# Performance work log

Hardware: AMD Instinct MI355X
Metric: run time of the kernel (lower is better)

Reference implementation:

```python
import jax, jax.numpy as jnp
import numpy as np

EMBED = 512
HEADS = 8
HEAD_DIM = EMBED // HEADS
MLP_HIDDEN = EMBED * 4
EPS = 1e-5


def _layernorm(x, g, b):
    mu = jnp.mean(x, axis=-1, keepdims=True)
    var = jnp.var(x, axis=-1, keepdims=True)
    return (x - mu) * jax.lax.rsqrt(var + EPS) * g + b


def setup_inputs() -> dict:
    key = jax.random.key(0)
    ks = jax.random.split(key, 12)
    s = 0.02
    return {
        "x": jax.random.normal(ks[0], (4, 2048, EMBED), dtype=jnp.float32),
        "ln1_g": jnp.ones((EMBED,), jnp.float32),
        "ln1_b": jnp.zeros((EMBED,), jnp.float32),
        "w_qkv": jax.random.normal(ks[1], (EMBED, 3 * EMBED), jnp.float32) * s,
        "b_qkv": jnp.zeros((3 * EMBED,), jnp.float32),
        "w_proj": jax.random.normal(ks[2], (EMBED, EMBED), jnp.float32) * s,
        "b_proj": jnp.zeros((EMBED,), jnp.float32),
        "ln2_g": jnp.ones((EMBED,), jnp.float32),
        "ln2_b": jnp.zeros((EMBED,), jnp.float32),
        "w1": jax.random.normal(ks[3], (EMBED, MLP_HIDDEN), jnp.float32) * s,
        "b1": jnp.zeros((MLP_HIDDEN,), jnp.float32),
        "w2": jax.random.normal(ks[4], (MLP_HIDDEN, EMBED), jnp.float32) * s,
        "b2": jnp.zeros((EMBED,), jnp.float32),
    }


def reference(x, ln1_g, ln1_b, w_qkv, b_qkv, w_proj, b_proj, ln2_g, ln2_b, w1, b1, w2, b2):
    B, N, C = x.shape
    scale = HEAD_DIM ** -0.5
    h = _layernorm(x, ln1_g, ln1_b)
    qkv = h @ w_qkv + b_qkv                       # [B,N,3C]
    qkv = qkv.reshape(B, N, 3, HEADS, HEAD_DIM)
    q = qkv[:, :, 0].transpose(0, 2, 1, 3)        # [B,H,N,D]
    k = qkv[:, :, 1].transpose(0, 2, 1, 3)
    v = qkv[:, :, 2].transpose(0, 2, 1, 3)
    attn = jnp.einsum('bhnd,bhmd->bhnm', q, k) * scale
    attn = jax.nn.softmax(attn, axis=-1)
    h = jnp.einsum('bhnm,bhmd->bhnd', attn, v)    # [B,H,N,D]
    h = h.transpose(0, 2, 1, 3).reshape(B, N, C)
    h = h @ w_proj + b_proj
    x = x + h
    m = _layernorm(x, ln2_g, ln2_b)
    m = jax.nn.gelu(m @ w1 + b1, approximate=False) @ w2 + b2
    return x + m
```

## Files before the change

kernel.cpp:

```cpp
#include <hip/hip_runtime.h>
#include <hip/hip_bf16.h>

typedef unsigned short u16;
typedef unsigned int u32;
typedef __attribute__((ext_vector_type(8))) __bf16 bf16x8;
typedef __attribute__((ext_vector_type(4))) float f32x4;
typedef __attribute__((ext_vector_type(16))) float f32x16;

#define LOG2E 1.4426950408889634f

__device__ __forceinline__ u16 f2bf(float f) {
  union { __hip_bfloat16 h; u16 u; } cv;
  cv.h = __float2bfloat16(f);
  return cv.u;
}

__device__ __forceinline__ float bf2f(u16 u) {
  union { u32 u; float f; } cv;
  cv.u = ((u32)u) << 16;
  return cv.f;
}

__device__ __forceinline__ u32 pk2(float a, float b) {
  return (u32)f2bf(a) | ((u32)f2bf(b) << 16);
}

#define EXP2 __builtin_amdgcn_exp2f

__device__ __forceinline__ f32x4 mfma16(bf16x8 a, bf16x8 b, f32x4 c) {
  return __builtin_amdgcn_mfma_f32_16x16x32_bf16(a, b, c, 0, 0, 0);
}
__device__ __forceinline__ f32x16 mfma32(bf16x8 a, bf16x8 b, f32x16 c) {
  return __builtin_amdgcn_mfma_f32_32x32x16_bf16(a, b, c, 0, 0, 0);
}

__device__ __forceinline__ void gload16(const u16* g, u16* lds) {
  __builtin_amdgcn_global_load_lds(
      (const __attribute__((address_space(1))) u32*)g,
      (__attribute__((address_space(3))) u32*)lds, 16, 0, 0);
}

__global__ __launch_bounds__(256) void prep_kernel(
    const float* __restrict__ w_qkv, u16* __restrict__ wqkvT,
    const float* __restrict__ w_proj, u16* __restrict__ wprojT,
    const float* __restrict__ w1, u16* __restrict__ w1T,
    const float* __restrict__ w2, u16* __restrict__ w2T,
    const float* __restrict__ X, const float* __restrict__ gam,
    const float* __restrict__ bet, u16* __restrict__ Y) {
  __shared__ float T[64][65];
  const int bid = blockIdx.x;
  if (bid < 768) {
    const float* W; u16* WT; int K, N, base;
    if (bid < 192)      { W = w_qkv; WT = wqkvT; K = 512;  N = 1536; base = 0; }
    else if (bid < 256) { W = w_proj; WT = wprojT; K = 512; N = 512; base = 192; }
    else if (bid < 512) { W = w1;   WT = w1T;   K = 512;  N = 2048; base = 256; }
    else                { W = w2;   WT = w2T;   K = 2048; N = 512;  base = 512; }
    int b = bid - base;
    int ntx = N >> 6;
    int bx = b % ntx, by = b / ntx;
    int tx = threadIdx.x & 63, ty = threadIdx.x >> 6;
#pragma unroll
    for (int i = 0; i < 64; i += 4)
      T[ty + i][tx] = W[(size_t)(by * 64 + ty + i) * N + bx * 64 + tx];
    __syncthreads();
#pragma unroll
    for (int i = 0; i < 64; i += 4)
      WT[(size_t)(bx * 64 + ty + i) * K + by * 64 + tx] = f2bf(T[tx][ty + i]);
  } else {
    int wid = threadIdx.x >> 6, l = threadIdx.x & 63;
    int row = (bid - 768) * 4 + wid;
    const float4* xp = reinterpret_cast<const float4*>(X + (size_t)row * 512);
    float4 a = xp[l], c = xp[l + 64];
    float s  = a.x + a.y + a.z + a.w + c.x + c.y + c.z + c.w;
    float s2 = a.x*a.x + a.y*a.y + a.z*a.z + a.w*a.w
             + c.x*c.x + c.y*c.y + c.z*c.z + c.w*c.w;
#pragma unroll
    for (int m = 1; m < 64; m <<= 1) { s += __shfl_xor(s, m); s2 += __shfl_xor(s2, m); }
    float mu = s * (1.f / 512.f);
    float rs = rsqrtf(s2 * (1.f / 512.f) - mu * mu + 1e-5f);
    const float4* gp = reinterpret_cast<const float4*>(gam);
    const float4* bp = reinterpret_cast<const float4*>(bet);
    float4 g0 = gp[l], g1 = gp[l + 64], b0 = bp[l], b1 = bp[l + 64];
    ushort4 o;
    o.x = f2bf((a.x - mu) * rs * g0.x + b0.x);
    o.y = f2bf((a.y - mu) * rs * g0.y + b0.y);
    o.z = f2bf((a.z - mu) * rs * g0.z + b0.z);
    o.w = f2bf((a.w - mu) * rs * g0.w + b0.w);
    reinterpret_cast<ushort4*>(Y + (size_t)row * 512)[l] = o;
    o.x = f2bf((c.x - mu) * rs * g1.x + b1.x);
    o.y = f2bf((c.y - mu) * rs * g1.y + b1.y);
    o.z = f2bf((c.z - mu) * rs * g1.z + b1.z);
    o.w = f2bf((c.w - mu) * rs * g1.w + b1.w);
    reinterpret_cast<ushort4*>(Y + (size_t)row * 512)[l + 64] = o;
  }
}

__global__ __launch_bounds__(256) void ln4_kernel(const float* __restrict__ X,
                                                  const float* __restrict__ gam,
                                                  const float* __restrict__ bet,
                                                  u16* __restrict__ Y) {
  int wid = threadIdx.x >> 6, l = threadIdx.x & 63;
  int row = blockIdx.x * 4 + wid;
  const float4* xp = reinterpret_cast<const float4*>(X + (size_t)row * 512);
  float4 a = xp[l], c = xp[l + 64];
  float s  = a.x + a.y + a.z + a.w + c.x + c.y + c.z + c.w;
  float s2 = a.x*a.x + a.y*a.y + a.z*a.z + a.w*a.w
           + c.x*c.x + c.y*c.y + c.z*c.z + c.w*c.w;
#pragma unroll
  for (int m = 1; m < 64; m <<= 1) { s += __shfl_xor(s, m); s2 += __shfl_xor(s2, m); }
  float mu = s * (1.f / 512.f);
  float rs = rsqrtf(s2 * (1.f / 512.f) - mu * mu + 1e-5f);
  const float4* gp = reinterpret_cast<const float4*>(gam);
  const float4* bp = reinterpret_cast<const float4*>(bet);
  float4 g0 = gp[l], g1 = gp[l + 64], b0 = bp[l], b1 = bp[l + 64];
  ushort4 o;
  o.x = f2bf((a.x - mu) * rs * g0.x + b0.x);
  o.y = f2bf((a.y - mu) * rs * g0.y + b0.y);
  o.z = f2bf((a.z - mu) * rs * g0.z + b0.z);
  o.w = f2bf((a.w - mu) * rs * g0.w + b0.w);
  reinterpret_cast<ushort4*>(Y + (size_t)row * 512)[l] = o;
  o.x = f2bf((c.x - mu) * rs * g1.x + b1.x);
  o.y = f2bf((c.y - mu) * rs * g1.y + b1.y);
  o.z = f2bf((c.z - mu) * rs * g1.z + b1.z);
  o.w = f2bf((c.w - mu) * rs * g1.w + b1.w);
  reinterpret_cast<ushort4*>(Y + (size_t)row * 512)[l + 64] = o;
}

template <int EPI>
__global__ __launch_bounds__(512)
__attribute__((amdgpu_waves_per_eu(4)))
void gemm_bt(const u16* __restrict__ A, const u16* __restrict__ BT,
             int M, int N, int K,
             const float* __restrict__ bias,
             u16* __restrict__ outU,
             u16* __restrict__ Qo, u16* __restrict__ Ko, u16* __restrict__ VTo) {
  constexpr int BM = 128, BN = 128, WC = 4, FM = 4;
  __shared__ u16 As[2][BM * 64];
  __shared__ u16 Bs[2][BN * 64];
  const int tid = threadIdx.x;
  const int wid = tid >> 6, l = tid & 63;
  const int lg = l >> 4, ll = l & 15;
  const int nx = gridDim.x;
  const int id = blockIdx.y * nx + blockIdx.x;
  const int cpx = (nx * gridDim.y) >> 3;
  const int wg = (id & 7) * cpx + (id >> 3);
  const int m0 = (wg / nx) * BM, n0 = (wg % nx) * BN;
  const int wm = (wid / WC) * (BM / 2), wn = (wid % WC) * 32;
  const f32x4 zf = {0.f, 0.f, 0.f, 0.f};
  f32x4 acc[FM][2];
#pragma unroll
  for (int i = 0; i < FM; i++) { acc[i][0] = zf; acc[i][1] = zf; }

  int srow[2], scol[2];
#pragma unroll
  for (int j = 0; j < 2; j++) {
    int p = j * 512 + tid;
    srow[j] = p >> 3;
    scol[j] = (p & 7) ^ (srow[j] & 7);
  }

  const int r0a = wm + ll;
  const int aoff0 = r0a * 64 + (lg ^ (r0a & 7)) * 8;
  const int r0b = wn + ll;
  const int boff0 = r0b * 64 + (lg ^ (r0b & 7)) * 8;

  auto stage = [&](int kt, int buf) {
#pragma unroll
    for (int j = 0; j < 2; j++) {
      int p = j * 512 + tid;
      gload16(A + (size_t)(m0 + srow[j]) * K + kt + scol[j] * 8, &As[buf][p * 8]);
      gload16(BT + (size_t)(n0 + srow[j]) * K + kt + scol[j] * 8, &Bs[buf][p * 8]);
    }
  };

  const int nt = K >> 6;
  stage(0, 0);
  for (int t = 0; t < nt; t++) {
    __syncthreads();
    if (t + 1 < nt) stage((t + 1) << 6, (t + 1) & 1);
    const u16* A_ = As[t & 1];
    const u16* B_ = Bs[t & 1];
#pragma unroll
    for (int kk = 0; kk < 2; kk++) {
      const int ax = kk ? (aoff0 ^ 32) : aoff0;
      const int bx = kk ? (boff0 ^ 32) : boff0;
      bf16x8 af[FM], bfr[2];
#pragma unroll
      for (int i = 0; i < FM; i++)
        af[i] = *reinterpret_cast<const bf16x8*>(A_ + ax + 1024 * i);
      bfr[0] = *reinterpret_cast<const bf16x8*>(B_ + bx);
      bfr[1] = *reinterpret_cast<const bf16x8*>(B_ + bx + 1024);
#pragma unroll
      for (int i = 0; i < FM; i++) {
        acc[i][0] = mfma16(af[i], bfr[0], acc[i][0]);
        acc[i][1] = mfma16(af[i], bfr[1], acc[i][1]);
      }
    }
  }

#pragma unroll
  for (int i = 0; i < FM; i++) {
#pragma unroll
    for (int j = 0; j < 2; j++) {
      int col = n0 + wn + j * 16 + ll;
      float bcol2 = bias[col];
      int rbase = m0 + wm + i * 16 + lg * 4;
      if (EPI == 0) {
        int bi = rbase >> 11, nseq0 = rbase & 2047;
        int t = col >> 9, rem = col & 511;
        int hh = rem >> 6, dd = rem & 63;
        if (t == 2) {
          ushort4 v;
          v.x = f2bf(acc[i][j][0] + bcol2);
          v.y = f2bf(acc[i][j][1] + bcol2);
          v.z = f2bf(acc[i][j][2] + bcol2);
          v.w = f2bf(acc[i][j][3] + bcol2);
          *reinterpret_cast<ushort4*>(
              VTo + ((size_t)((bi << 3) + hh) * 64 + dd) * 2048 + nseq0) = v;
        } else {
          size_t hidx = ((size_t)((bi << 3) + hh) * 2048 + nseq0) * 64 + dd;
#pragma unroll
          for (int r = 0; r < 4; r++) {
            float val = acc[i][j][r] + bcol2;
            if (t == 0) Qo[hidx + (size_t)r * 64] = f2bf(val * (0.125f * LOG2E));
            else        Ko[hidx + (size_t)r * 64] = f2bf(val);
          }
        }
      } else {
#pragma unroll
        for (int r = 0; r < 4; r++) {
          float val = acc[i][j][r] + bcol2;
          float y = 0.7978845608f * (val + 0.044715f * val * val * val);
          float e = EXP2(2.0f * LOG2E * y);
          float t2 = 1.0f - 2.0f / (e + 1.0f);
          outU[(size_t)(rbase + r) * 2048 + col] = f2bf(0.5f * val * (1.0f + t2));
        }
      }
    }
  }
}

__global__ __launch_bounds__(256)
__attribute__((amdgpu_waves_per_eu(4)))
void gemm_bt64(const u16* __restrict__ A, const u16* __restrict__ BT,
               int M, int N, int K,
               const float* __restrict__ bias,
               const float* __restrict__ resid,
               float* __restrict__ outF) {
  __shared__ u16 As[2][64 * 64];
  __shared__ u16 Bs[2][64 * 64];
  const int tid = threadIdx.x;
  const int wid = tid >> 6, l = tid & 63;
  const int lg = l >> 4, ll = l & 15;
  const int nx = gridDim.x;
  const int id = blockIdx.y * nx + blockIdx.x;
  const int cpx = (nx * gridDim.y) >> 3;
  const int wg = (id & 7) * cpx + (id >> 3);
  const int m0 = (wg / nx) * 64, n0 = (wg % nx) * 64;
  const int wm = (wid >> 1) * 32, wn = (wid & 1) * 32;
  const f32x4 zf = {0.f, 0.f, 0.f, 0.f};
  f32x4 acc[2][2];
  acc[0][0] = zf; acc[0][1] = zf; acc[1][0] = zf; acc[1][1] = zf;

  int srow[2], scol[2];
#pragma unroll
  for (int j = 0; j < 2; j++) {
    int p = j * 256 + tid;
    srow[j] = p >> 3;
    scol[j] = (p & 7) ^ (srow[j] & 7);
  }

  const int ra = wm + ll;
  const int aoff0 = ra * 64 + (lg ^ (ra & 7)) * 8;
  const int rb = wn + ll;
  const int boff0 = rb * 64 + (lg ^ (rb & 7)) * 8;

  auto stage = [&](int kt, int buf) {
#pragma unroll
    for (int j = 0; j < 2; j++) {
      int p = j * 256 + tid;
      gload16(A + (size_t)(m0 + srow[j]) * K + kt + scol[j] * 8, &As[buf][p * 8]);
      gload16(BT + (size_t)(n0 + srow[j]) * K + kt + scol[j] * 8, &Bs[buf][p * 8]);
    }
  };

  const int nt = K >> 6;
  stage(0, 0);
  for (int t = 0; t < nt; t++) {
    __syncthreads();
    if (t + 1 < nt) stage((t + 1) << 6, (t + 1) & 1);
    const u16* A_ = As[t & 1];
    const u16* B_ = Bs[t & 1];
#pragma unroll
    for (int kk = 0; kk < 2; kk++) {
      const int ax = kk ? (aoff0 ^ 32) : aoff0;
      const int bx = kk ? (boff0 ^ 32) : boff0;
      bf16x8 a0 = *reinterpret_cast<const bf16x8*>(A_ + ax);
      bf16x8 a1 = *reinterpret_cast<const bf16x8*>(A_ + ax + 1024);
      bf16x8 b0 = *reinterpret_cast<const bf16x8*>(B_ + bx);
      bf16x8 b1 = *reinterpret_cast<const bf16x8*>(B_ + bx + 1024);
      acc[0][0] = mfma16(a0, b0, acc[0][0]);
      acc[0][1] = mfma16(a0, b1, acc[0][1]);
      acc[1][0] = mfma16(a1, b0, acc[1][0]);
      acc[1][1] = mfma16(a1, b1, acc[1][1]);
    }
  }

#pragma unroll
  for (int i = 0; i < 2; i++) {
#pragma unroll
    for (int j = 0; j < 2; j++) {
      int col = n0 + wn + j * 16 + ll;
      float bcol2 = bias[col];
      int rbase = m0 + wm + i * 16 + lg * 4;
#pragma unroll
      for (int r = 0; r < 4; r++) {
        size_t idx = (size_t)(rbase + r) * 512 + col;
        outF[idx] = acc[i][j][r] + bcol2 + resid[idx];
      }
    }
  }
}

__global__ __launch_bounds__(256)
__attribute__((amdgpu_waves_per_eu(4)))
void attn_kernel(const u16* __restrict__ Q,
                 const u16* __restrict__ Kt,
                 const u16* __restrict__ VT,
                 u16* __restrict__ Opart,
                 float* __restrict__ Stat) {
  __shared__ __align__(16) u16 Kbuf[2][64 * 64];
  __shared__ __align__(16) u16 Vbuf[2][64 * 64];
  const int tid = threadIdx.x;
  const int wid = tid >> 6, l = tid & 63;
  const int lq = l & 31, h = l >> 5;
  const int b = blockIdx.z, hd = blockIdx.y;
  const int qt = blockIdx.x >> 1, sp = blockIdx.x & 1;
  const int qbase = qt * 128 + wid * 32;
  const int kv0 = sp * 1024;
  const size_t hoff = (size_t)(b * 8 + hd) * 2048 * 64;
  const u16* Qh = Q + hoff;
  const u16* Kh = Kt + hoff;
  const u16* Vh = VT + hoff;

  bf16x8 qf[4];
#pragma unroll
  for (int s = 0; s < 4; s++)
    qf[s] = *reinterpret_cast<const bf16x8*>(Qh + (size_t)(qbase + lq) * 64 + s * 16 + h * 8);

  int koff[4];
#pragma unroll
  for (int s = 0; s < 4; s++)
    koff[s] = (lq * 8 + ((s * 2 + h) ^ (lq & 7))) * 8;

  f32x16 oacc[2];
#pragma unroll
  for (int r = 0; r < 16; r++) { oacc[0][r] = 0.f; oacc[1][r] = 0.f; }
  float ps0 = 0.f, ps1 = 0.f;

  auto stage = [&](int kb, int buf) {
#pragma unroll
    for (int half = 0; half < 2; half++) {
      int g0 = half * 256 + wid * 64;
      int p = g0 + l;
      int row = p >> 3;
      int c = (p & 7) ^ (row & 7);
      gload16(Kh + (size_t)(kb + row) * 64 + c * 8, &Kbuf[buf][g0 * 8]);
      gload16(Vh + (size_t)row * 2048 + kb + c * 8, &Vbuf[buf][g0 * 8]);
    }
  };

  stage(kv0, 0);
  for (int i = 0; i < 16; i++) {
    __syncthreads();
    if (i < 15) stage(kv0 + (i + 1) * 64, (i + 1) & 1);
    const u16* Kc = Kbuf[i & 1];
    const u16* Vc = Vbuf[i & 1];

#pragma unroll
    for (int t = 0; t < 2; t++) {
      f32x16 st;
#pragma unroll
      for (int r = 0; r < 16; r++) st[r] = 0.f;
      __builtin_amdgcn_s_setprio(1);
      if (t == 0) {
#pragma unroll
        for (int s = 0; s < 4; s++)
          st = mfma32(*reinterpret_cast<const bf16x8*>(Kc + koff[s]), qf[s], st);
      } else {
#pragma unroll
        for (int s = 0; s < 4; s++)
          st = mfma32(*reinterpret_cast<const bf16x8*>(Kc + koff[s] + 2048), qf[s], st);
      }
      __builtin_amdgcn_s_setprio(0);

#pragma unroll
      for (int j = 0; j < 16; j += 4) {
        float p0 = EXP2(st[j + 0]);
        float p1 = EXP2(st[j + 1]);
        float p2 = EXP2(st[j + 2]);
        float p3 = EXP2(st[j + 3]);
        st[j + 0] = p0; st[j + 1] = p1; st[j + 2] = p2; st[j + 3] = p3;
        ps0 += p0 + p2; ps1 += p1 + p3;
      }

      u32 w0 = pk2(st[0], st[1]),   w1 = pk2(st[2], st[3]);
      u32 w2 = pk2(st[4], st[5]),   w3 = pk2(st[6], st[7]);
      u32 w4 = pk2(st[8], st[9]),   w5 = pk2(st[10], st[11]);
      u32 w6 = pk2(st[12], st[13]), w7 = pk2(st[14], st[15]);
      uint4 pa0, pa1;
#if __has_builtin(__builtin_amdgcn_permlane32_swap)
      auto r02 = __builtin_amdgcn_permlane32_swap(w0, w2, false, false);
      auto r13 = __builtin_amdgcn_permlane32_swap(w1, w3, false, false);
      auto r46 = __builtin_amdgcn_permlane32_swap(w4, w6, false, false);
      auto r57 = __builtin_amdgcn_permlane32_swap(w5, w7, false, false);
      pa0.x = (u32)r02[0]; pa0.y = (u32)r13[0]; pa0.z = (u32)r02[1]; pa0.w = (u32)r13[1];
      pa1.x = (u32)r46[0]; pa1.y = (u32)r57[0]; pa1.z = (u32)r46[1]; pa1.w = (u32)r57[1];
#else
      u32 ra2, rb2;
      ra2 = (u32)__shfl_xor((int)(h ? w0 : w2), 32);
      rb2 = (u32)__shfl_xor((int)(h ? w1 : w3), 32);
      pa0.x = h ? ra2 : w0; pa0.y = h ? rb2 : w1;
      pa0.z = h ? w0 : ra2; pa0.w = h ? w1 : rb2;
      ra2 = (u32)__shfl_xor((int)(h ? w4 : w6), 32);
      rb2 = (u32)__shfl_xor((int)(h ? w5 : w7), 32);
      pa1.x = h ? ra2 : w4; pa1.y = h ? rb2 : w5;
      pa1.z = h ? w4 : ra2; pa1.w = h ? w5 : rb2;
#endif
      union { uint4 u; bf16x8 v; } p0u, p1u;
      p0u.u = pa0; p1u.u = pa1;
      __builtin_amdgcn_s_setprio(1);
      if (t == 0) {
        oacc[0] = mfma32(p0u.v, *reinterpret_cast<const bf16x8*>(Vc + koff[0]), oacc[0]);
        oacc[0] = mfma32(p1u.v, *reinterpret_cast<const bf16x8*>(Vc + koff[1]), oacc[0]);
        oacc[1] = mfma32(p0u.v, *reinterpret_cast<const bf16x8*>(Vc + koff[0] + 2048), oacc[1]);
        oacc[1] = mfma32(p1u.v, *reinterpret_cast<const bf16x8*>(Vc + koff[1] + 2048), oacc[1]);
      } else {
        oacc[0] = mfma32(p0u.v, *reinterpret_cast<const bf16x8*>(Vc + koff[2]), oacc[0]);
        oacc[0] = mfma32(p1u.v, *reinterpret_cast<const bf16x8*>(Vc + koff[3]), oacc[0]);
        oacc[1] = mfma32(p0u.v, *reinterpret_cast<const bf16x8*>(Vc + koff[2] + 2048), oacc[1]);
        oacc[1] = mfma32(p1u.v, *reinterpret_cast<const bf16x8*>(Vc + koff[3] + 2048), oacc[1]);
      }
      __builtin_amdgcn_s_setprio(0);
    }
  }

  float lsum = ps0 + ps1;
  lsum += __shfl_xor(lsum, 32);

  u16* Op = Opart + (size_t)sp * 8192 * 512;
#pragma unroll
  for (int r = 0; r < 16; r++) {
    const int qr = (r & 3) + 8 * (r >> 2) + 4 * h;
    size_t row = (size_t)b * 2048 + qbase + qr;
#pragma unroll
    for (int dt = 0; dt < 2; dt++) {
      int col = hd * 64 + dt * 32 + lq;
      Op[row * 512 + col] = f2bf(oacc[dt][r]);
    }
  }
  if (h == 0)
    Stat[(size_t)sp * 32 * 2048 + (size_t)(b * 8 + hd) * 2048 + qbase + lq] = lsum;
}

__global__ __launch_bounds__(256) void attn_merge(const u16* __restrict__ Opart,
                                                  const float* __restrict__ Stat,
                                                  u16* __restrict__ O) {
  int gid = blockIdx.x * 256 + threadIdx.x;
  int row = gid >> 6;
  int c8 = (gid & 63) * 8;
  int hd = c8 >> 6;
  int bh = (row >> 11) * 8 + hd;
  int n = row & 2047;
  float L = Stat[(size_t)bh * 2048 + n] +
            Stat[(size_t)32 * 2048 + (size_t)bh * 2048 + n];
  float acc[8];
#pragma unroll
  for (int j = 0; j < 8; j++) acc[j] = 0.f;
#pragma unroll
  for (int p = 0; p < 2; p++) {
    const ushort4* pp = reinterpret_cast<const ushort4*>(
        Opart + (size_t)p * 8192 * 512 + (size_t)row * 512 + c8);
    ushort4 v0 = pp[0], v1 = pp[1];
    acc[0] += bf2f(v0.x); acc[1] += bf2f(v0.y);
    acc[2] += bf2f(v0.z); acc[3] += bf2f(v0.w);
    acc[4] += bf2f(v1.x); acc[5] += bf2f(v1.y);
    acc[6] += bf2f(v1.z); acc[7] += bf2f(v1.w);
  }
  float li = 1.0f / L;
  ushort4 o0, o1;
  o0.x = f2bf(acc[0] * li); o0.y = f2bf(acc[1] * li);
  o0.z = f2bf(acc[2] * li); o0.w = f2bf(acc[3] * li);
  o1.x = f2bf(acc[4] * li); o1.y = f2bf(acc[5] * li);
  o1.z = f2bf(acc[6] * li); o1.w = f2bf(acc[7] * li);
  ushort4* op = reinterpret_cast<ushort4*>(O + (size_t)row * 512 + c8);
  op[0] = o0;
  op[1] = o1;
}

extern "C" void kernel_launch(void* const* d_in, const int* in_sizes, int n_in,
                              void* d_out, int out_size, void* d_ws, size_t ws_size,
                              hipStream_t stream) {
  const float* x      = (const float*)d_in[0];
  const float* ln1_g  = (const float*)d_in[1];
  const float* ln1_b  = (const float*)d_in[2];
  const float* w_qkv  = (const float*)d_in[3];
  const float* b_qkv  = (const float*)d_in[4];
  const float* w_proj = (const float*)d_in[5];
  const float* b_proj = (const float*)d_in[6];
  const float* ln2_g  = (const float*)d_in[7];
  const float* ln2_b  = (const float*)d_in[8];
  const float* w1     = (const float*)d_in[9];
  const float* b1     = (const float*)d_in[10];
  const float* w2     = (const float*)d_in[11];
  const float* b2     = (const float*)d_in[12];
  float* out = (float*)d_out;

  const int M = 8192;
  char* w = (char*)d_ws;
  u16* wqkvT  = (u16*)w; w += (size_t)1536 * 512 * 2;
  u16* wprojT = (u16*)w; w += (size_t)512 * 512 * 2;
  u16* w1T    = (u16*)w; w += (size_t)2048 * 512 * 2;
  u16* w2T    = (u16*)w; w += (size_t)512 * 2048 * 2;
  u16* h1     = (u16*)w; w += (size_t)M * 512 * 2;
  u16* Qb     = (u16*)w; w += (size_t)M * 512 * 2;
  u16* Kb     = (u16*)w; w += (size_t)M * 512 * 2;
  u16* VTb    = (u16*)w; w += (size_t)M * 512 * 2;
  u16* attn   = (u16*)w; w += (size_t)M * 512 * 2;
  u16* h2     = (u16*)w; w += (size_t)M * 512 * 2;
  u16* mid    = (u16*)w; w += (size_t)M * 2048 * 2;
  float* Stat = (float*)w; w += (size_t)2 * 32 * 2048 * sizeof(float);
  u16* Opart = (u16*)mid;

  prep_kernel<<<2816, 256, 0, stream>>>(w_qkv, wqkvT, w_proj, wprojT,
                                        w1, w1T, w2, w2T,
                                        x, ln1_g, ln1_b, h1);

  gemm_bt<0><<<dim3(1536 / 128, M / 128), 512, 0, stream>>>(
      h1, wqkvT, M, 1536, 512, b_qkv, nullptr, Qb, Kb, VTb);

  attn_kernel<<<dim3(32, 8, 4), 256, 0, stream>>>(Qb, Kb, VTb, Opart, Stat);
  attn_merge<<<M * 64 / 256, 256, 0, stream>>>(Opart, Stat, attn);

  gemm_bt64<<<dim3(512 / 64, M / 64), 256, 0, stream>>>(
      attn, wprojT, M, 512, 512, b_proj, x, out);

  ln4_kernel<<<M / 4, 256, 0, stream>>>(out, ln2_g, ln2_b, h2);

  gemm_bt<2><<<dim3(2048 / 128, M / 128), 512, 0, stream>>>(
      h2, w1T, M, 2048, 512, b1, mid, nullptr, nullptr, nullptr);

  gemm_bt64<<<dim3(512 / 64, M / 64), 256, 0, stream>>>(
      mid, w2T, M, 512, 2048, b2, out, out);
}
```

Baseline: 161.4 us.

## Fuse split-attention merge into output projection GEMM A-operand load

```diff
diff --git a/kernel.cpp b/kernel.cpp
--- a/kernel.cpp
+++ b/kernel.cpp
@@ -38,6 +38,15 @@
   __builtin_amdgcn_global_load_lds(
       (const __attribute__((address_space(1))) u32*)g,
       (__attribute__((address_space(3))) u32*)lds, 16, 0, 0);
+}
+
+__device__ __forceinline__ bf16x8 merge8(bf16x8 a, bf16x8 b, float li) {
+  union { bf16x8 v; u16 e[8]; } ua, ub, uo;
+  ua.v = a; ub.v = b;
+#pragma unroll
+  for (int i = 0; i < 8; i++)
+    uo.e[i] = f2bf((bf2f(ua.e[i]) + bf2f(ub.e[i])) * li);
+  return uo.v;
 }
 
 __global__ __launch_bounds__(256) void prep_kernel(
@@ -235,6 +244,105 @@
           float t2 = 1.0f - 2.0f / (e + 1.0f);
           outU[(size_t)(rbase + r) * 2048 + col] = f2bf(0.5f * val * (1.0f + t2));
         }
+      }
+    }
+  }
+}
+
+__global__ __launch_bounds__(256)
+__attribute__((amdgpu_waves_per_eu(4)))
+void proj_fused(const u16* __restrict__ Opart, const float* __restrict__ Stat,
+                const u16* __restrict__ BT,
+                const float* __restrict__ bias,
+                const float* __restrict__ resid,
+                float* __restrict__ outF) {
+  __shared__ u16 As0[2][64 * 64];
+  __shared__ u16 As1[2][64 * 64];
+  __shared__ u16 Bs[2][64 * 64];
+  const int tid = threadIdx.x;
+  const int wid = tid >> 6, l = tid & 63;
+  const int lg = l >> 4, ll = l & 15;
+  const int nx = gridDim.x;
+  const int id = blockIdx.y * nx + blockIdx.x;
+  const int cpx = (nx * gridDim.y) >> 3;
+  const int wg = (id & 7) * cpx + (id >> 3);
+  const int m0 = (wg / nx) * 64, n0 = (wg % nx) * 64;
+  const int wm = (wid >> 1) * 32, wn = (wid & 1) * 32;
+  const f32x4 zf = {0.f, 0.f, 0.f, 0.f};
+  f32x4 acc[2][2];
+  acc[0][0] = zf; acc[0][1] = zf; acc[1][0] = zf; acc[1][1] = zf;
+
+  int srow[2], scol[2];
+#pragma unroll
+  for (int j = 0; j < 2; j++) {
+    int p = j * 256 + tid;
+    srow[j] = p >> 3;
+    scol[j] = (p & 7) ^ (srow[j] & 7);
+  }
+
+  const int ra = wm + ll;
+  const int aoff0 = ra * 64 + (lg ^ (ra & 7)) * 8;
+  const int rb = wn + ll;
+  const int boff0 = rb * 64 + (lg ^ (rb & 7)) * 8;
+
+  const int row0 = m0 + ra;
+  const int bb8 = (row0 >> 11) * 8;
+  const int n0r = row0 & 2047;
+  float linv0[8], linv1[8];
+#pragma unroll
+  for (int hh = 0; hh < 8; hh++) {
+    size_t s0 = (size_t)(bb8 + hh) * 2048 + n0r;
+    linv0[hh] = 1.0f / (Stat[s0] + Stat[65536 + s0]);
+    linv1[hh] = 1.0f / (Stat[s0 + 16] + Stat[65536 + s0 + 16]);
+  }
+
+  auto stage = [&](int kt, int buf) {
+#pragma unroll
+    for (int j = 0; j < 2; j++) {
+      int p = j * 256 + tid;
+      size_t aidx = (size_t)(m0 + srow[j]) * 512 + kt + scol[j] * 8;
+      gload16(Opart + aidx, &As0[buf][p * 8]);
+      gload16(Opart + (size_t)8192 * 512 + aidx, &As1[buf][p * 8]);
+      gload16(BT + (size_t)(n0 + srow[j]) * 512 + kt + scol[j] * 8, &Bs[buf][p * 8]);
+    }
+  };
+
+  stage(0, 0);
+#pragma unroll
+  for (int t = 0; t < 8; t++) {
+    __syncthreads();
+    if (t + 1 < 8) stage((t + 1) << 6, (t + 1) & 1);
+    const u16* A0_ = As0[t & 1];
+    const u16* A1_ = As1[t & 1];
+    const u16* B_ = Bs[t & 1];
+#pragma unroll
+    for (int kk = 0; kk < 2; kk++) {
+      const int ax = kk ? (aoff0 ^ 32) : aoff0;
+      const int bx = kk ? (boff0 ^ 32) : boff0;
+      bf16x8 a0 = merge8(*reinterpret_cast<const bf16x8*>(A0_ + ax),
+                         *reinterpret_cast<const bf16x8*>(A1_ + ax), linv0[t]);
+      bf16x8 a1 = merge8(*reinterpret_cast<const bf16x8*>(A0_ + ax + 1024),
+                         *reinterpret_cast<const bf16x8*>(A1_ + ax + 1024), linv1[t]);
+      bf16x8 b0 = *reinterpret_cast<const bf16x8*>(B_ + bx);
+      bf16x8 b1 = *reinterpret_cast<const bf16x8*>(B_ + bx + 1024);
+      acc[0][0] = mfma16(a0, b0, acc[0][0]);
+      acc[0][1] = mfma16(a0, b1, acc[0][1]);
+      acc[1][0] = mfma16(a1, b0, acc[1][0]);
+      acc[1][1] = mfma16(a1, b1, acc[1][1]);
+    }
+  }
+
+#pragma unroll
+  for (int i = 0; i < 2; i++) {
+#pragma unroll
+    for (int j = 0; j < 2; j++) {
+      int col = n0 + wn + j * 16 + ll;
+      float bcol2 = bias[col];
+      int rbase = m0 + wm + i * 16 + lg * 4;
+#pragma unroll
+      for (int r = 0; r < 4; r++) {
+        size_t idx = (size_t)(rbase + r) * 512 + col;
+        outF[idx] = acc[i][j][r] + bcol2 + resid[idx];
       }
     }
   }
@@ -463,41 +571,6 @@
     Stat[(size_t)sp * 32 * 2048 + (size_t)(b * 8 + hd) * 2048 + qbase + lq] = lsum;
 }
 
-__global__ __launch_bounds__(256) void attn_merge(const u16* __restrict__ Opart,
-                                                  const float* __restrict__ Stat,
-                                                  u16* __restrict__ O) {
-  int gid = blockIdx.x * 256 + threadIdx.x;
-  int row = gid >> 6;
-  int c8 = (gid & 63) * 8;
-  int hd = c8 >> 6;
-  int bh = (row >> 11) * 8 + hd;
-  int n = row & 2047;
-  float L = Stat[(size_t)bh * 2048 + n] +
-            Stat[(size_t)32 * 2048 + (size_t)bh * 2048 + n];
-  float acc[8];
-#pragma unroll
-  for (int j = 0; j < 8; j++) acc[j] = 0.f;
-#pragma unroll
-  for (int p = 0; p < 2; p++) {
-    const ushort4* pp = reinterpret_cast<const ushort4*>(
-        Opart + (size_t)p * 8192 * 512 + (size_t)row * 512 + c8);
-    ushort4 v0 = pp[0], v1 = pp[1];
-    acc[0] += bf2f(v0.x); acc[1] += bf2f(v0.y);
-    acc[2] += bf2f(v0.z); acc[3] += bf2f(v0.w);
-    acc[4] += bf2f(v1.x); acc[5] += bf2f(v1.y);
-    acc[6] += bf2f(v1.z); acc[7] += bf2f(v1.w);
-  }
-  float li = 1.0f / L;
-  ushort4 o0, o1;
-  o0.x = f2bf(acc[0] * li); o0.y = f2bf(acc[1] * li);
-  o0.z = f2bf(acc[2] * li); o0.w = f2bf(acc[3] * li);
-  o1.x = f2bf(acc[4] * li); o1.y = f2bf(acc[5] * li);
-  o1.z = f2bf(acc[6] * li); o1.w = f2bf(acc[7] * li);
-  ushort4* op = reinterpret_cast<ushort4*>(O + (size_t)row * 512 + c8);
-  op[0] = o0;
-  op[1] = o1;
-}
-
 extern "C" void kernel_launch(void* const* d_in, const int* in_sizes, int n_in,
                               void* d_out, int out_size, void* d_ws, size_t ws_size,
                               hipStream_t stream) {
@@ -540,10 +613,9 @@
       h1, wqkvT, M, 1536, 512, b_qkv, nullptr, Qb, Kb, VTb);
 
   attn_kernel<<<dim3(32, 8, 4), 256, 0, stream>>>(Qb, Kb, VTb, Opart, Stat);
-  attn_merge<<<M * 64 / 256, 256, 0, stream>>>(Opart, Stat, attn);
-
-  gemm_bt64<<<dim3(512 / 64, M / 64), 256, 0, stream>>>(
-      attn, wprojT, M, 512, 512, b_proj, x, out);
+
+  proj_fused<<<dim3(512 / 64, M / 64), 256, 0, stream>>>(
+      Opart, Stat, wprojT, b_proj, x, out);
 
   ln4_kernel<<<M / 4, 256, 0, stream>>>(out, ln2_g, ln2_b, h2);
 
```

Measured after the change: 170.3 us. 1.06x slower.
